# Kernel optimization log

Hardware: AMD Instinct MI355X
Metric: run time of the kernel (lower is better)

The kernel has to match this reference:

```python
import jax, jax.numpy as jnp
import numpy as np

B, QLEN, EMBED = 16, 64, 4096
N_HEADS, N_KV, HEAD_DIM = 32, 8, 128
PAST = 4032
MASK_VAL = -66504.0  # value used by IPEXTransformerAtten causal mask


def _rotate_half(x):
    x1, x2 = jnp.split(x, 2, axis=-1)
    return jnp.concatenate([-x2, x1], axis=-1)


def setup_inputs() -> dict:
    key = jax.random.key(0)
    ks = jax.random.split(key, 8)
    s = 0.02
    return {
        "hidden_states": jax.random.normal(ks[0], (B, QLEN, EMBED), jnp.float32),
        "past_key": jax.random.normal(ks[1], (B, N_KV, PAST, HEAD_DIM), jnp.float32),
        "past_value": jax.random.normal(ks[2], (B, N_KV, PAST, HEAD_DIM), jnp.float32),
        "q_wei": jax.random.normal(ks[3], (EMBED, N_HEADS * HEAD_DIM), jnp.float32) * s,
        "k_wei": jax.random.normal(ks[4], (EMBED, N_KV * HEAD_DIM), jnp.float32) * s,
        "v_wei": jax.random.normal(ks[5], (EMBED, N_KV * HEAD_DIM), jnp.float32) * s,
        "out_wei": jax.random.normal(ks[6], (N_HEADS * HEAD_DIM, EMBED), jnp.float32) * s,
        "beam_idx": jax.random.randint(ks[7], (B,), 0, B, jnp.int32),
    }


def reference(hidden_states, past_key, past_value, q_wei, k_wei, v_wei, out_wei, beam_idx):
    b, s, e = hidden_states.shape
    n_kv, past_len, d = past_key.shape[1], past_key.shape[2], past_key.shape[3]
    n_h = q_wei.shape[1] // d
    g = n_h // n_kv  # num_key_value_groups

    # QKV projections (weights stored [in, out], matching torch.matmul(hidden, wei))
    q = (hidden_states @ q_wei).reshape(b, s, n_h, d)
    k = (hidden_states @ k_wei).reshape(b, s, n_kv, d)
    v = (hidden_states @ v_wei).reshape(b, s, n_kv, d)

    # rotary embedding (GPT-NeoX style, full head_dim) at positions past_len..past_len+s
    pos = (past_len + jnp.arange(s)).astype(jnp.float32)
    inv_freq = 1.0 / (10000.0 ** (jnp.arange(0, d, 2, dtype=jnp.float32) / d))
    freqs = pos[:, None] * inv_freq[None, :]
    emb = jnp.concatenate([freqs, freqs], axis=-1)
    cos = jnp.cos(emb)[None, :, None, :].astype(hidden_states.dtype)
    sin = jnp.sin(emb)[None, :, None, :].astype(hidden_states.dtype)
    q = q * cos + _rotate_half(q) * sin
    k = k * cos + _rotate_half(k) * sin

    # beam reorder of KV cache (gather along batch-beam dim), then append new kv
    pk = past_key[beam_idx]   # [b, n_kv, past, d]
    pv = past_value[beam_idx]
    k_all = jnp.concatenate([pk, k.transpose(0, 2, 1, 3)], axis=2)  # [b, n_kv, T, d]
    v_all = jnp.concatenate([pv, v.transpose(0, 2, 1, 3)], axis=2)
    T = past_len + s

    # grouped-query attention
    qh = q.transpose(0, 2, 1, 3).reshape(b, n_kv, g, s, d)
    scores = jnp.einsum('bkgsd,bktd->bkgst', qh, k_all) / jnp.sqrt(jnp.asarray(d, hidden_states.dtype))
    causal = jnp.arange(T)[None, :] <= (past_len + jnp.arange(s))[:, None]  # [s, T]
    scores = jnp.where(causal[None, None, None], scores, MASK_VAL)
    probs = jax.nn.softmax(scores, axis=-1)
    ctx = jnp.einsum('bkgst,bktd->bkgsd', probs, v_all)
    ctx = ctx.reshape(b, n_h, s, d).transpose(0, 2, 1, 3).reshape(b, s, n_h * d)
    return ctx @ out_wei
```

## Files before the change

### kernel.cpp

```cpp
#include <hip/hip_runtime.h>
#include <stdint.h>

#define DEVFN __device__ __forceinline__

typedef unsigned short u16;
typedef unsigned int u32;

using f32x4 = __attribute__((ext_vector_type(4))) float;
using bfv8  = __attribute__((ext_vector_type(8))) short;
using s16x4 = __attribute__((ext_vector_type(4))) short;

#define CSC 0.12751745f

DEVFN u16 f2bf(float f){
  u32 u = __float_as_uint(f);
  u32 r = u + 0x7FFFu + ((u >> 16) & 1u);
  return (u16)(r >> 16);
}
DEVFN float bf2f(u16 h){ return __uint_as_float(((u32)h) << 16); }

DEVFN void llds16(const void* g, void* l){
  __builtin_amdgcn_global_load_lds((const __attribute__((address_space(1))) void*)g,
                                   (__attribute__((address_space(3))) void*)l, 16, 0, 0);
}

DEVFN bfv8 as_bf(uint4 v){ return __builtin_bit_cast(bfv8, v); }

#if __has_builtin(__builtin_amdgcn_mfma_f32_16x16x16bf16_1k)
DEVFN f32x4 mfma16(s16x4 a, s16x4 b, f32x4 c){
  return __builtin_amdgcn_mfma_f32_16x16x16bf16_1k(a, b, c, 0, 0, 0);
}
#else
DEVFN f32x4 mfma16(s16x4 a, s16x4 b, f32x4 c){
  asm("v_mfma_f32_16x16x16_bf16 %0, %1, %2, %0" : "+v"(c) : "v"(a), "v"(b));
  return c;
}
#endif

DEVFN u32 cvtpk(float lo, float hi){
  u32 w;
  asm("v_cvt_pk_bf16_f32 %0, %1, %2" : "=v"(w) : "v"(lo), "v"(hi));
  return w;
}

__global__ __launch_bounds__(256) void cvt_hid_kernel(const float* __restrict__ src, u16* __restrict__ dst){
  int i = blockIdx.x * 256 + threadIdx.x;
  const float* s = src + (size_t)i * 8;
  float4 a = *(const float4*)s;
  float4 b = *(const float4*)(s + 4);
  u16 t[8] = {f2bf(a.x), f2bf(a.y), f2bf(a.z), f2bf(a.w),
              f2bf(b.x), f2bf(b.y), f2bf(b.z), f2bf(b.w)};
  *(uint4*)(dst + (size_t)i * 8) = *(const uint4*)t;
}

__global__ __launch_bounds__(256) void wtrans_kernel(const float* __restrict__ qw, const float* __restrict__ kw,
                                                     const float* __restrict__ vw, const float* __restrict__ ow,
                                                     u16* __restrict__ wtall, u16* __restrict__ wto){
  __shared__ float tile[64 * 65];
  int z = blockIdx.x, tid = threadIdx.x;
  const float* W; u16* WT; int Ndim; int rz;
  if (z < 4096)      { W = qw; WT = wtall;                         Ndim = 4096; rz = z; }
  else if (z < 5120) { W = kw; WT = wtall + (size_t)4096 * 4096;   Ndim = 1024; rz = z - 4096; }
  else if (z < 6144) { W = vw; WT = wtall + (size_t)5120 * 4096;   Ndim = 1024; rz = z - 5120; }
  else               { W = ow; WT = wto;                           Ndim = 4096; rz = z - 6144; }
  int ntn = Ndim >> 6;
  int tk = rz / ntn, tn = rz % ntn;
  const float* src = W + (size_t)(tk * 64) * Ndim + tn * 64;
  #pragma unroll
  for (int it = 0; it < 4; ++it){
    int fi = tid + it * 256;
    int r = fi >> 4, c4 = (fi & 15) * 4;
    float4 v = *(const float4*)(src + (size_t)r * Ndim + c4);
    tile[r * 65 + c4 + 0] = v.x; tile[r * 65 + c4 + 1] = v.y;
    tile[r * 65 + c4 + 2] = v.z; tile[r * 65 + c4 + 3] = v.w;
  }
  __syncthreads();
  u16* dst = WT + (size_t)(tn * 64) * 4096 + tk * 64;
  #pragma unroll
  for (int it = 0; it < 2; ++it){
    int ci = tid + it * 256;
    int n = ci >> 3, k8 = (ci & 7) * 8;
    u16 tmp[8];
    #pragma unroll
    for (int j = 0; j < 8; ++j) tmp[j] = f2bf(tile[(k8 + j) * 65 + n]);
    *(uint4*)(dst + (size_t)n * 4096 + k8) = *(const uint4*)tmp;
  }
}

template<int OUTF32>
__global__ __launch_bounds__(256) void gemm_kernel(const u16* __restrict__ A, const u16* __restrict__ BT,
                                                   void* __restrict__ Cv, int N, int ntn){
  constexpr int K = 4096;
  __shared__ u16 As[2][128 * 32];
  __shared__ u16 Bs[2][128 * 32];
  int bid = blockIdx.x;
  int bm = bid / ntn, bn = bid % ntn;
  int tid = threadIdx.x, lane = tid & 63, w = tid >> 6;
  int wr = w >> 1, wc = w & 1;
  int l15 = lane & 15, lh = lane >> 4;
  const u16* Ab = A  + (size_t)(bm * 128) * K;
  const u16* Bb = BT + (size_t)(bn * 128) * K;
  f32x4 acc[4][4];
  #pragma unroll
  for (int m = 0; m < 4; ++m)
    #pragma unroll
    for (int n = 0; n < 4; ++n) acc[m][n] = f32x4{0.f, 0.f, 0.f, 0.f};

  auto stage = [&](int buf, int k0){
    #pragma unroll
    for (int p = 0; p < 2; ++p){
      int cid = tid + p * 256;
      int row = cid >> 2, k8 = (cid & 3) * 8;
      llds16(Ab + (size_t)row * K + k0 + k8, (char*)(&As[buf][0]) + p * 4096 + w * 1024);
      llds16(Bb + (size_t)row * K + k0 + k8, (char*)(&Bs[buf][0]) + p * 4096 + w * 1024);
    }
  };
  stage(0, 0);
  __syncthreads();
  for (int kt = 0; kt < K / 32; ++kt){
    int cur = kt & 1;
    if (kt + 1 < K / 32) stage(cur ^ 1, (kt + 1) * 32);
    uint4 af[4], bfr[4];
    #pragma unroll
    for (int i = 0; i < 4; ++i){
      af[i]  = *(const uint4*)(&As[cur][(wr * 64 + i * 16 + l15) * 32 + lh * 8]);
      bfr[i] = *(const uint4*)(&Bs[cur][(wc * 64 + i * 16 + l15) * 32 + lh * 8]);
    }
    #pragma unroll
    for (int m = 0; m < 4; ++m)
      #pragma unroll
      for (int n = 0; n < 4; ++n)
        acc[m][n] = __builtin_amdgcn_mfma_f32_16x16x32_bf16(as_bf(af[m]), as_bf(bfr[n]), acc[m][n], 0, 0, 0);
    __syncthreads();
  }
  int row0 = bm * 128 + wr * 64, col0 = bn * 128 + wc * 64;
  if (OUTF32){
    float* C = (float*)Cv;
    #pragma unroll
    for (int m = 0; m < 4; ++m)
      #pragma unroll
      for (int n = 0; n < 4; ++n)
        #pragma unroll
        for (int r = 0; r < 4; ++r)
          C[(size_t)(row0 + m * 16 + lh * 4 + r) * N + col0 + n * 16 + l15] = acc[m][n][r];
  } else {
    u16* C = (u16*)Cv;
    #pragma unroll
    for (int m = 0; m < 4; ++m)
      #pragma unroll
      for (int n = 0; n < 4; ++n)
        #pragma unroll
        for (int r = 0; r < 4; ++r)
          C[(size_t)(row0 + m * 16 + lh * 4 + r) * N + col0 + n * 16 + l15] = f2bf(acc[m][n][r]);
  }
}

__global__ __launch_bounds__(256) void rope_kernel(const u16* __restrict__ qkvp, u16* __restrict__ qrope,
                                                   float* __restrict__ knew, float* __restrict__ vnew){
  int z = blockIdx.x, tid = threadIdx.x;
  if (z < 512){
    int b = z >> 5, h = z & 31;
    u16* dst = qrope + (size_t)((b * 32 + h) * 64) * 128;
    for (int it = 0; it < 16; ++it){
      int i = tid + it * 256;
      int s = i >> 6, j = i & 63;
      const u16* src = qkvp + (size_t)(b * 64 + s) * 6144 + h * 128;
      float q0 = bf2f(src[j]), q1 = bf2f(src[j + 64]);
      float inv = expf(-(float)j * 0.14391157f);
      float ang = (4032.0f + (float)s) * inv;
      float sn = sinf(ang), cs = cosf(ang);
      int dcs = ((j >> 3) ^ s) & 7;
      dst[s * 128 + dcs * 8 + (j & 7)]      = f2bf((q0 * cs - q1 * sn) * CSC);
      dst[s * 128 + 64 + dcs * 8 + (j & 7)] = f2bf((q1 * cs + q0 * sn) * CSC);
    }
  } else {
    int z2 = z - 512, b = z2 >> 3, kvh = z2 & 7;
    for (int it = 0; it < 16; ++it){
      int i = tid + it * 256;
      int s = i >> 6, j = i & 63;
      const u16* src = qkvp + (size_t)(b * 64 + s) * 6144 + 4096 + kvh * 128;
      float q0 = bf2f(src[j]), q1 = bf2f(src[j + 64]);
      float inv = expf(-(float)j * 0.14391157f);
      float ang = (4032.0f + (float)s) * inv;
      float sn = sinf(ang), cs = cosf(ang);
      float* kd = knew + ((size_t)(b * 8 + kvh) * 64 + s) * 128;
      kd[j]      = q0 * cs - q1 * sn;
      kd[j + 64] = q1 * cs + q0 * sn;
      const u16* vs = qkvp + (size_t)(b * 64 + s) * 6144 + 5120 + kvh * 128;
      float* vd = vnew + ((size_t)(b * 8 + kvh) * 64 + s) * 128;
      vd[j]      = bf2f(vs[j]);
      vd[j + 64] = bf2f(vs[j + 64]);
    }
  }
}

__global__ __launch_bounds__(512, 2) void attn_kernel(const u16* __restrict__ qrope, const float* __restrict__ pastk,
                                                      const float* __restrict__ pastv, const float* __restrict__ knew,
                                                      const float* __restrict__ vnew, const int* __restrict__ beam,
                                                      float* __restrict__ pctx, float* __restrict__ pm,
                                                      float* __restrict__ pl){
  __shared__ u16 Qs[4][8192];
  __shared__ u16 Ks[2][4096];
  __shared__ u16 Vs[2][4608];
  int kv = blockIdx.x, b = blockIdx.y, chunk = blockIdx.z;
  int tid = threadIdx.x, lane = tid & 63, w = tid >> 6;
  int l15 = lane & 15, lh = lane >> 4;
  constexpr int NT = 64;

  if (w >= 4){
    int p = w - 4;
    int dblk = l15;
    int tq = p * 8 + lh * 2;
    int bmb = beam[b];
    const float* kpast = pastk + (size_t)(bmb * 8 + kv) * 4032 * 128;
    const float* vpast = pastv + (size_t)(bmb * 8 + kv) * 4032 * 128;
    const float* knb = knew + (size_t)(b * 8 + kv) * 64 * 128;
    const float* vnb = vnew + (size_t)(b * 8 + kv) * 64 * 128;

    auto loadTile = [&](int tix, float4* rk, float4* rv){
      int tg0 = chunk * 2048 + tix * 32;
      const float *ksrc, *vsrc;
      if (tg0 >= 4032){ ksrc = knb + (size_t)(tg0 - 4032) * 128; vsrc = vnb + (size_t)(tg0 - 4032) * 128; }
      else            { ksrc = kpast + (size_t)tg0 * 128;         vsrc = vpast + (size_t)tg0 * 128; }
      const float* k0 = ksrc + (size_t)tq * 128 + dblk * 8;
      const float* k1 = ksrc + (size_t)(tq + 1) * 128 + dblk * 8;
      const float* v0 = vsrc + (size_t)tq * 128 + dblk * 8;
      const float* v1 = vsrc + (size_t)(tq + 1) * 128 + dblk * 8;
      rk[0] = *(const float4*)k0; rk[1] = *(const float4*)(k0 + 4);
      rk[2] = *(const float4*)k1; rk[3] = *(const float4*)(k1 + 4);
      rv[0] = *(const float4*)v0; rv[1] = *(const float4*)(v0 + 4);
      rv[2] = *(const float4*)v1; rv[3] = *(const float4*)(v1 + 4);
    };
    auto writeTile = [&](int buf, const float4* rk, const float4* rv){
      uint4 pk0, pk1;
      pk0.x = cvtpk(rk[0].x, rk[0].y); pk0.y = cvtpk(rk[0].z, rk[0].w);
      pk0.z = cvtpk(rk[1].x, rk[1].y); pk0.w = cvtpk(rk[1].z, rk[1].w);
      pk1.x = cvtpk(rk[2].x, rk[2].y); pk1.y = cvtpk(rk[2].z, rk[2].w);
      pk1.z = cvtpk(rk[3].x, rk[3].y); pk1.w = cvtpk(rk[3].z, rk[3].w);
      int dcs0 = (dblk & 8) | ((dblk ^ tq) & 7);
      int dcs1 = (dblk & 8) | ((dblk ^ (tq + 1)) & 7);
      *(uint4*)(&Ks[buf][tq * 128 + dcs0 * 8])       = pk0;
      *(uint4*)(&Ks[buf][(tq + 1) * 128 + dcs1 * 8]) = pk1;
      float va[8] = {rv[0].x, rv[0].y, rv[0].z, rv[0].w, rv[1].x, rv[1].y, rv[1].z, rv[1].w};
      float vb[8] = {rv[2].x, rv[2].y, rv[2].z, rv[2].w, rv[3].x, rv[3].y, rv[3].z, rv[3].w};
      #pragma unroll
      for (int dd = 0; dd < 8; ++dd){
        int d = dblk * 8 + dd;
        int cc = (p ^ ((dblk ^ dd) & 3) ^ (dblk >> 2)) & 3;
        *(u32*)(&Vs[buf][d * 36 + cc * 8 + lh * 2]) = cvtpk(va[dd], vb[dd]);
      }
    };

    float4 rkA[4], rvA[4], rkB[4], rvB[4];
    loadTile(0, rkA, rvA);
    asm volatile("s_waitcnt vmcnt(0)" ::: "memory");
    writeTile(0, rkA, rvA);
    loadTile(1, rkB, rvB);
    asm volatile("s_waitcnt lgkmcnt(0)" ::: "memory");
    __builtin_amdgcn_sched_barrier(0);
    __builtin_amdgcn_s_barrier();
    __builtin_amdgcn_sched_barrier(0);
    for (int it = 0; it < NT; it += 2){
      if (it + 1 < NT){
        asm volatile("s_waitcnt vmcnt(0)" ::: "memory");
        writeTile(1, rkB, rvB);
        if (it + 2 < NT) loadTile(it + 2, rkA, rvA);
        asm volatile("s_waitcnt lgkmcnt(0)" ::: "memory");
      }
      __builtin_amdgcn_sched_barrier(0);
      __builtin_amdgcn_s_barrier();
      __builtin_amdgcn_sched_barrier(0);
      if (it + 2 < NT){
        asm volatile("s_waitcnt vmcnt(0)" ::: "memory");
        writeTile(0, rkA, rvA);
        if (it + 3 < NT) loadTile(it + 3, rkB, rvB);
        asm volatile("s_waitcnt lgkmcnt(0)" ::: "memory");
      }
      __builtin_amdgcn_sched_barrier(0);
      __builtin_amdgcn_s_barrier();
      __builtin_amdgcn_sched_barrier(0);
    }
    return;
  }

  const u16* qb = qrope + (size_t)((b * 32 + kv * 4 + w) * 64) * 128;
  #pragma unroll
  for (int c = 0; c < 16; ++c)
    llds16((const char*)qb + c * 1024 + lane * 16, (char*)(&Qs[w][0]) + c * 1024);
  asm volatile("s_waitcnt vmcnt(0)" ::: "memory");

  f32x4 cacc[8][4];
  float mrow[4], lrow[4];
  #pragma unroll
  for (int qm = 0; qm < 4; ++qm){ mrow[qm] = -3.0e38f; lrow[qm] = 0.f; }
  #pragma unroll
  for (int nd = 0; nd < 8; ++nd)
    #pragma unroll
    for (int qm = 0; qm < 4; ++qm) cacc[nd][qm] = f32x4{0.f, 0.f, 0.f, 0.f};

  __builtin_amdgcn_sched_barrier(0);
  __builtin_amdgcn_s_barrier();
  __builtin_amdgcn_sched_barrier(0);

  for (int it = 0; it < NT; ++it){
    const u16* Kc = &Ks[it & 1][0];
    const u16* Vc = &Vs[it & 1][0];

    f32x4 sacc[2][4];
    #pragma unroll
    for (int tt = 0; tt < 2; ++tt)
      #pragma unroll
      for (int qm = 0; qm < 4; ++qm) sacc[tt][qm] = f32x4{0.f, 0.f, 0.f, 0.f};
    #pragma unroll
    for (int ks = 0; ks < 4; ++ks){
      int dc = ks * 4 + lh;
      int dcs = (dc & 8) | ((dc ^ l15) & 7);
      uint4 kf0 = *(const uint4*)(Kc + l15 * 128 + dcs * 8);
      uint4 kf1 = *(const uint4*)(Kc + (16 + l15) * 128 + dcs * 8);
      #pragma unroll
      for (int qm = 0; qm < 4; ++qm){
        uint4 qf = *(const uint4*)(&Qs[w][(qm * 16 + l15) * 128 + dcs * 8]);
        sacc[0][qm] = __builtin_amdgcn_mfma_f32_16x16x32_bf16(as_bf(kf0), as_bf(qf), sacc[0][qm], 0, 0, 0);
        sacc[1][qm] = __builtin_amdgcn_mfma_f32_16x16x32_bf16(as_bf(kf1), as_bf(qf), sacc[1][qm], 0, 0, 0);
      }
    }

    if (chunk == 1 && it >= 62){
      int toff = (it - 62) * 32;
      #pragma unroll
      for (int tt = 0; tt < 2; ++tt)
        #pragma unroll
        for (int qm = 0; qm < 4; ++qm)
          #pragma unroll
          for (int r = 0; r < 4; ++r){
            int t = toff + tt * 16 + lh * 4 + r;
            int q = qm * 16 + l15;
            if (t > q) sacc[tt][qm][r] = -3.0e38f;
          }
    }

    #pragma unroll
    for (int qm = 0; qm < 4; ++qm){
      float rm = sacc[0][qm][0];
      #pragma unroll
      for (int tt = 0; tt < 2; ++tt)
        #pragma unroll
        for (int r = 0; r < 4; ++r) rm = fmaxf(rm, sacc[tt][qm][r]);
      if (__any(rm > mrow[qm] + 8.0f)){
        rm = fmaxf(rm, __shfl_xor(rm, 16));
        rm = fmaxf(rm, __shfl_xor(rm, 32));
        float mn = fmaxf(mrow[qm], rm);
        float esc = exp2f(mrow[qm] - mn);
        mrow[qm] = mn;
        lrow[qm] *= esc;
        #pragma unroll
        for (int nd = 0; nd < 8; ++nd) cacc[nd][qm] *= esc;
      }
      float s = 0.f;
      #pragma unroll
      for (int tt = 0; tt < 2; ++tt)
        #pragma unroll
        for (int r = 0; r < 4; ++r){
          float pp = exp2f(sacc[tt][qm][r] - mrow[qm]);
          sacc[tt][qm][r] = pp;
          s += pp;
        }
      lrow[qm] += s;
    }

    #pragma unroll
    for (int tt = 0; tt < 2; ++tt){
      s16x4 pa[4];
      #pragma unroll
      for (int qm = 0; qm < 4; ++qm){
        uint2 u;
        u.x = cvtpk(sacc[tt][qm][0], sacc[tt][qm][1]);
        u.y = cvtpk(sacc[tt][qm][2], sacc[tt][qm][3]);
        pa[qm] = __builtin_bit_cast(s16x4, u);
      }
      #pragma unroll
      for (int nd = 0; nd < 8; ++nd){
        int swzv = ((nd * 2) ^ (l15 >> 3) ^ l15) & 3;
        int cc = ((tt * 2 + (lh >> 1)) ^ swzv ^ (nd >> 1)) & 3;
        uint2 vr = *(const uint2*)(Vc + (nd * 16 + l15) * 36 + cc * 8 + (lh & 1) * 4);
        s16x4 vfr = __builtin_bit_cast(s16x4, vr);
        #pragma unroll
        for (int qm = 0; qm < 4; ++qm)
          cacc[nd][qm] = mfma16(vfr, pa[qm], cacc[nd][qm]);
      }
    }
    __builtin_amdgcn_sched_barrier(0);
    __builtin_amdgcn_s_barrier();
    __builtin_amdgcn_sched_barrier(0);
  }

  #pragma unroll
  for (int qm = 0; qm < 4; ++qm){
    lrow[qm] += __shfl_xor(lrow[qm], 16);
    lrow[qm] += __shfl_xor(lrow[qm], 32);
  }

  float* pc = pctx + (size_t)(((chunk * 16 + b) * 8 + kv) * 4 + w) * 8192;
  #pragma unroll
  for (int qm = 0; qm < 4; ++qm){
    int q = qm * 16 + l15;
    #pragma unroll
    for (int nd = 0; nd < 8; ++nd)
      *(f32x4*)(pc + (size_t)q * 128 + nd * 16 + lh * 4) = cacc[nd][qm];
  }
  if (lh == 0){
    size_t mb = (size_t)((chunk * 16 + b) * 8 + kv) * 256 + w * 64;
    #pragma unroll
    for (int qm = 0; qm < 4; ++qm){
      pm[mb + qm * 16 + l15] = mrow[qm];
      pl[mb + qm * 16 + l15] = lrow[qm];
    }
  }
}

__global__ __launch_bounds__(256) void combine_kernel(const float* __restrict__ pctx, const float* __restrict__ pm,
                                                      const float* __restrict__ pl, u16* __restrict__ ctxb){
  int z = blockIdx.x;
  int g = z & 3, kv = (z >> 2) & 7, b = z >> 5;
  int tid = threadIdx.x;
  int s = tid >> 2, dq = (tid & 3) * 32;
  float mv[2], lv[2];
  #pragma unroll
  for (int c = 0; c < 2; ++c){
    size_t mi = (size_t)((c * 16 + b) * 8 + kv) * 256 + g * 64 + s;
    mv[c] = pm[mi]; lv[c] = pl[mi];
  }
  float M = fmaxf(mv[0], mv[1]);
  float wc[2], wsum = 0.f;
  #pragma unroll
  for (int c = 0; c < 2; ++c){ wc[c] = exp2f(mv[c] - M); wsum += wc[c] * lv[c]; }
  float inv = 1.0f / wsum;
  u16* dst = ctxb + (size_t)(b * 64 + s) * 4096 + (kv * 4 + g) * 128 + dq;
  #pragma unroll
  for (int j4 = 0; j4 < 8; ++j4){
    float4 a = {0.f, 0.f, 0.f, 0.f};
    #pragma unroll
    for (int c = 0; c < 2; ++c){
      const float* p = pctx + (size_t)(((c * 16 + b) * 8 + kv) * 4 + g) * 8192 + s * 128 + dq + j4 * 4;
      float4 v = *(const float4*)p;
      a.x += wc[c] * v.x; a.y += wc[c] * v.y; a.z += wc[c] * v.z; a.w += wc[c] * v.w;
    }
    u16 t4[4] = {f2bf(a.x * inv), f2bf(a.y * inv), f2bf(a.z * inv), f2bf(a.w * inv)};
    *(uint2*)(dst + j4 * 4) = *(const uint2*)t4;
  }
}

extern "C" void kernel_launch(void* const* d_in, const int* in_sizes, int n_in,
                              void* d_out, int out_size, void* d_ws, size_t ws_size,
                              hipStream_t stream){
  const float* hidden = (const float*)d_in[0];
  const float* pastk  = (const float*)d_in[1];
  const float* pastv  = (const float*)d_in[2];
  const float* qw     = (const float*)d_in[3];
  const float* kw     = (const float*)d_in[4];
  const float* vw     = (const float*)d_in[5];
  const float* ow     = (const float*)d_in[6];
  const int*   beam   = (const int*)d_in[7];

  char* ws = (char*)d_ws;
  size_t off = 0;
  auto alloc = [&](size_t sz){ char* p = ws + off; off += sz; return p; };
  u16*   wtall = (u16*)alloc(50331648);
  u16*   wto   = (u16*)alloc(33554432);
  u16*   hidb  = (u16*)alloc(8388608);
  u16*   qkvp  = (u16*)alloc(12582912);
  u16*   qrope = (u16*)alloc(8388608);
  float* knew  = (float*)alloc(4194304);
  float* vnew  = (float*)alloc(4194304);
  float* pctx  = (float*)alloc(33554432);
  float* pm    = (float*)alloc(262144);
  float* pl    = (float*)alloc(262144);
  u16*   ctxb  = (u16*)alloc(8388608);
  if (off > ws_size) return;

  cvt_hid_kernel<<<2048, 256, 0, stream>>>(hidden, hidb);
  wtrans_kernel<<<10240, 256, 0, stream>>>(qw, kw, vw, ow, wtall, wto);
  gemm_kernel<0><<<384, 256, 0, stream>>>(hidb, wtall, (void*)qkvp, 6144, 48);
  rope_kernel<<<640, 256, 0, stream>>>(qkvp, qrope, knew, vnew);
  attn_kernel<<<dim3(8, 16, 2), 512, 0, stream>>>(qrope, pastk, pastv, knew, vnew, beam, pctx, pm, pl);
  combine_kernel<<<512, 256, 0, stream>>>(pctx, pm, pl, ctxb);
  gemm_kernel<1><<<256, 256, 0, stream>>>(ctxb, wto, d_out, 4096, 32);
}
```

Before: 425.5 us.

## Split attention heads across blocks and remap GEMM block ids per XCD

The attention kernel now splits each kv-group's four query heads across two 256-thread blocks (2 compute + 2 loader waves) instead of one 512-thread block, doubling the grid. Each loader wave now fetches four K/V rows per tile instead of two. The split is meant to raise the number of blocks and occupancy, at the cost of loading and converting each past K/V tile twice from global memory. Separately, the GEMM remaps block ids so consecutive tiles land on the same XCD, which should improve L2 reuse.

Result: slower. 459.3 us (+8.0%).

```diff
diff --git a/kernel.cpp b/kernel.cpp
--- a/kernel.cpp
+++ b/kernel.cpp
@@ -94,6 +94,10 @@
   __shared__ u16 As[2][128 * 32];
   __shared__ u16 Bs[2][128 * 32];
   int bid = blockIdx.x;
+  {
+    int cpx = gridDim.x >> 3;
+    bid = (bid & 7) * cpx + (bid >> 3);
+  }
   int bm = bid / ntn, bn = bid % ntn;
   int tid = threadIdx.x, lane = tid & 63, w = tid >> 6;
   int wr = w >> 1, wc = w & 1;
@@ -194,23 +198,24 @@
   }
 }
 
-__global__ __launch_bounds__(512, 2) void attn_kernel(const u16* __restrict__ qrope, const float* __restrict__ pastk,
+__global__ __launch_bounds__(256, 2) void attn_kernel(const u16* __restrict__ qrope, const float* __restrict__ pastk,
                                                       const float* __restrict__ pastv, const float* __restrict__ knew,
                                                       const float* __restrict__ vnew, const int* __restrict__ beam,
                                                       float* __restrict__ pctx, float* __restrict__ pm,
                                                       float* __restrict__ pl){
-  __shared__ u16 Qs[4][8192];
+  __shared__ u16 Qs[2][8192];
   __shared__ u16 Ks[2][4096];
   __shared__ u16 Vs[2][4608];
-  int kv = blockIdx.x, b = blockIdx.y, chunk = blockIdx.z;
+  int kv = blockIdx.x, b = blockIdx.y;
+  int chunk = blockIdx.z >> 1, hp = blockIdx.z & 1;
   int tid = threadIdx.x, lane = tid & 63, w = tid >> 6;
   int l15 = lane & 15, lh = lane >> 4;
   constexpr int NT = 64;
 
-  if (w >= 4){
-    int p = w - 4;
+  if (w >= 2){
+    int p = w - 2;
     int dblk = l15;
-    int tq = p * 8 + lh * 2;
+    int tq = p * 16 + lh * 4;
     int bmb = beam[b];
     const float* kpast = pastk + (size_t)(bmb * 8 + kv) * 4032 * 128;
     const float* vpast = pastv + (size_t)(bmb * 8 + kv) * 4032 * 128;
@@ -222,36 +227,40 @@
       const float *ksrc, *vsrc;
       if (tg0 >= 4032){ ksrc = knb + (size_t)(tg0 - 4032) * 128; vsrc = vnb + (size_t)(tg0 - 4032) * 128; }
       else            { ksrc = kpast + (size_t)tg0 * 128;         vsrc = vpast + (size_t)tg0 * 128; }
-      const float* k0 = ksrc + (size_t)tq * 128 + dblk * 8;
-      const float* k1 = ksrc + (size_t)(tq + 1) * 128 + dblk * 8;
-      const float* v0 = vsrc + (size_t)tq * 128 + dblk * 8;
-      const float* v1 = vsrc + (size_t)(tq + 1) * 128 + dblk * 8;
-      rk[0] = *(const float4*)k0; rk[1] = *(const float4*)(k0 + 4);
-      rk[2] = *(const float4*)k1; rk[3] = *(const float4*)(k1 + 4);
-      rv[0] = *(const float4*)v0; rv[1] = *(const float4*)(v0 + 4);
-      rv[2] = *(const float4*)v1; rv[3] = *(const float4*)(v1 + 4);
+      #pragma unroll
+      for (int j = 0; j < 4; ++j){
+        const float* kp = ksrc + (size_t)(tq + j) * 128 + dblk * 8;
+        const float* vp = vsrc + (size_t)(tq + j) * 128 + dblk * 8;
+        rk[2 * j]     = *(const float4*)kp; rk[2 * j + 1] = *(const float4*)(kp + 4);
+        rv[2 * j]     = *(const float4*)vp; rv[2 * j + 1] = *(const float4*)(vp + 4);
+      }
     };
     auto writeTile = [&](int buf, const float4* rk, const float4* rv){
-      uint4 pk0, pk1;
-      pk0.x = cvtpk(rk[0].x, rk[0].y); pk0.y = cvtpk(rk[0].z, rk[0].w);
-      pk0.z = cvtpk(rk[1].x, rk[1].y); pk0.w = cvtpk(rk[1].z, rk[1].w);
-      pk1.x = cvtpk(rk[2].x, rk[2].y); pk1.y = cvtpk(rk[2].z, rk[2].w);
-      pk1.z = cvtpk(rk[3].x, rk[3].y); pk1.w = cvtpk(rk[3].z, rk[3].w);
-      int dcs0 = (dblk & 8) | ((dblk ^ tq) & 7);
-      int dcs1 = (dblk & 8) | ((dblk ^ (tq + 1)) & 7);
-      *(uint4*)(&Ks[buf][tq * 128 + dcs0 * 8])       = pk0;
-      *(uint4*)(&Ks[buf][(tq + 1) * 128 + dcs1 * 8]) = pk1;
-      float va[8] = {rv[0].x, rv[0].y, rv[0].z, rv[0].w, rv[1].x, rv[1].y, rv[1].z, rv[1].w};
-      float vb[8] = {rv[2].x, rv[2].y, rv[2].z, rv[2].w, rv[3].x, rv[3].y, rv[3].z, rv[3].w};
+      #pragma unroll
+      for (int j = 0; j < 4; ++j){
+        uint4 pk;
+        pk.x = cvtpk(rk[2 * j].x, rk[2 * j].y);         pk.y = cvtpk(rk[2 * j].z, rk[2 * j].w);
+        pk.z = cvtpk(rk[2 * j + 1].x, rk[2 * j + 1].y); pk.w = cvtpk(rk[2 * j + 1].z, rk[2 * j + 1].w);
+        int t = tq + j;
+        int dcs = (dblk & 8) | ((dblk ^ t) & 7);
+        *(uint4*)(&Ks[buf][t * 128 + dcs * 8]) = pk;
+      }
+      int c0 = 2 * p + (lh >> 1);
+      int bi = (lh & 1) * 4;
+      const float* vf = (const float*)rv;
       #pragma unroll
       for (int dd = 0; dd < 8; ++dd){
         int d = dblk * 8 + dd;
-        int cc = (p ^ ((dblk ^ dd) & 3) ^ (dblk >> 2)) & 3;
-        *(u32*)(&Vs[buf][d * 36 + cc * 8 + lh * 2]) = cvtpk(va[dd], vb[dd]);
+        int ccs = (c0 ^ ((dblk ^ dd) & 3) ^ (dblk >> 2)) & 3;
+        u32 w0 = cvtpk(vf[dd], vf[8 + dd]);
+        u32 w1 = cvtpk(vf[16 + dd], vf[24 + dd]);
+        u16* vd = &Vs[buf][d * 36 + ccs * 8 + bi];
+        *(u32*)vd = w0;
+        *(u32*)(vd + 2) = w1;
       }
     };
 
-    float4 rkA[4], rvA[4], rkB[4], rvB[4];
+    float4 rkA[8], rvA[8], rkB[8], rvB[8];
     loadTile(0, rkA, rvA);
     asm volatile("s_waitcnt vmcnt(0)" ::: "memory");
     writeTile(0, rkA, rvA);
@@ -283,7 +292,8 @@
     return;
   }
 
-  const u16* qb = qrope + (size_t)((b * 32 + kv * 4 + w) * 64) * 128;
+  int head = hp * 2 + w;
+  const u16* qb = qrope + (size_t)((b * 32 + kv * 4 + head) * 64) * 128;
   #pragma unroll
   for (int c = 0; c < 16; ++c)
     llds16((const char*)qb + c * 1024 + lane * 16, (char*)(&Qs[w][0]) + c * 1024);
@@ -400,7 +410,7 @@
     lrow[qm] += __shfl_xor(lrow[qm], 32);
   }
 
-  float* pc = pctx + (size_t)(((chunk * 16 + b) * 8 + kv) * 4 + w) * 8192;
+  float* pc = pctx + (size_t)(((chunk * 16 + b) * 8 + kv) * 4 + head) * 8192;
   #pragma unroll
   for (int qm = 0; qm < 4; ++qm){
     int q = qm * 16 + l15;
@@ -409,7 +419,7 @@
       *(f32x4*)(pc + (size_t)q * 128 + nd * 16 + lh * 4) = cacc[nd][qm];
   }
   if (lh == 0){
-    size_t mb = (size_t)((chunk * 16 + b) * 8 + kv) * 256 + w * 64;
+    size_t mb = (size_t)((chunk * 16 + b) * 8 + kv) * 256 + head * 64;
     #pragma unroll
     for (int qm = 0; qm < 4; ++qm){
       pm[mb + qm * 16 + l15] = mrow[qm];
@@ -482,7 +492,7 @@
   wtrans_kernel<<<10240, 256, 0, stream>>>(qw, kw, vw, ow, wtall, wto);
   gemm_kernel<0><<<384, 256, 0, stream>>>(hidb, wtall, (void*)qkvp, 6144, 48);
   rope_kernel<<<640, 256, 0, stream>>>(qkvp, qrope, knew, vnew);
-  attn_kernel<<<dim3(8, 16, 2), 512, 0, stream>>>(qrope, pastk, pastv, knew, vnew, beam, pctx, pm, pl);
+  attn_kernel<<<dim3(8, 16, 4), 256, 0, stream>>>(qrope, pastk, pastv, knew, vnew, beam, pctx, pm, pl);
   combine_kernel<<<512, 256, 0, stream>>>(pctx, pm, pl, ctxb);
   gemm_kernel<1><<<256, 256, 0, stream>>>(ctxb, wto, d_out, 4096, 32);
 }
```
